# Kernel optimization log

Hardware: AMD Instinct MI355X
Metric: run time of the kernel (lower is better)

## Reference

```python
import jax, jax.numpy as jnp
import numpy as np

LATENT = 256
MID = 512
T = 5          # num_transforms
OUT = T * 6 + T  # 35
THRESH = 0.9   # MATRIX_NORM_THRESHOLD
EPS = 1e-5     # torch LayerNorm eps
B = 131072


def _xavier(key, fan_in, fan_out):
    lim = np.sqrt(6.0 / (fan_in + fan_out)).astype(np.float32)
    return jax.random.uniform(key, (fan_in, fan_out), jnp.float32, -lim, lim)


def setup_inputs() -> dict:
    key = jax.random.key(0)
    ks = jax.random.split(key, 8)
    z = jax.random.normal(ks[0], (B, LATENT), jnp.float32)
    W1 = _xavier(ks[1], LATENT, MID)
    Wa = _xavier(ks[2], MID, MID)
    Wb = _xavier(ks[3], MID, MID)
    Wout = _xavier(ks[4], MID, OUT)
    bias = lambda n: jnp.full((n,), 0.01, jnp.float32)  # nn.init.constant_(bias, 0.01)
    return {
        "z": z,
        "W1": W1, "b1": bias(MID), "g1": jnp.ones((MID,), jnp.float32), "be1": jnp.zeros((MID,), jnp.float32),
        "Wa": Wa, "ba": bias(MID), "ga": jnp.ones((MID,), jnp.float32), "bea": jnp.zeros((MID,), jnp.float32),
        "Wb": Wb, "bb": bias(MID), "gb": jnp.ones((MID,), jnp.float32), "beb": jnp.zeros((MID,), jnp.float32),
        "Wout": Wout, "bout": bias(OUT),
    }


def _layernorm(x, g, b):
    mu = jnp.mean(x, axis=-1, keepdims=True)
    var = jnp.mean(jnp.square(x - mu), axis=-1, keepdims=True)
    return (x - mu) * jax.lax.rsqrt(var + EPS) * g + b


def reference(z, W1, b1, g1, be1, Wa, ba, ga, bea, Wb, bb, gb, beb, Wout, bout):
    # Linear -> LayerNorm -> ReLU
    h = jax.nn.relu(_layernorm(z @ W1 + b1, g1, be1))
    # ResidualBlock: Linear -> LN -> SiLU -> Linear -> LN, then skip add
    y = jax.nn.silu(_layernorm(h @ Wa + ba, ga, bea))
    y = _layernorm(y @ Wb + bb, gb, beb)
    h = h + y
    x = h @ Wout + bout                     # [B, 35]

    affines = x[:, : T * 6].reshape(-1, T, 2, 3)  # [B, T, 2, 3]
    logits = x[:, T * 6:]                         # [B, T]
    probs = jax.nn.softmax(logits, axis=-1)

    M = affines[..., :2]                          # [B, T, 2, 2]
    U, S, Vh = jnp.linalg.svd(M, full_matrices=False)
    Sc = jnp.minimum(S, THRESH)                   # clamp(max=0.9)
    M2 = jnp.einsum("btij,btj,btjk->btik", U, Sc, Vh)
    affines = jnp.concatenate([M2, affines[..., 2:]], axis=-1)
    return affines, probs
```

## Files before the change

### kernel.cpp

```cpp
#include <hip/hip_runtime.h>
#include <hip/hip_bf16.h>

#define BQ     131072
#define NT     5

typedef unsigned short u16;
typedef unsigned int   u32;
typedef unsigned long long u64;
typedef __attribute__((ext_vector_type(8))) short bf16x8;
typedef __attribute__((ext_vector_type(4))) float f32x4;
typedef __attribute__((ext_vector_type(2))) float f32x2;

__device__ __forceinline__ u16 f2bf(float x) {
  union { float f; u32 u; } v; v.f = x;
  u32 r = (v.u + 0x7FFFu + ((v.u >> 16) & 1u)) >> 16;
  return (u16)r;
}

__global__ __launch_bounds__(256) void transpose_cast(
    const float* __restrict__ src, u16* __restrict__ dst, int K, int N, int NP) {
  __shared__ float tile[32][33];
  int kx = blockIdx.x * 32, ny = blockIdx.y * 32;
  int tx = threadIdx.x, ty = threadIdx.y;
#pragma unroll
  for (int i = 0; i < 4; i++) {
    int k = kx + ty + i * 8, n = ny + tx;
    tile[ty + i * 8][tx] = (k < K && n < N) ? src[(size_t)k * N + n] : 0.f;
  }
  __syncthreads();
#pragma unroll
  for (int i = 0; i < 4; i++) {
    int n = ny + ty + i * 8, k = kx + tx;
    if (n < NP && k < K) dst[(size_t)n * K + k] = f2bf(tile[tx][ty + i * 8]);
  }
}

template <int K, int ACT>
__device__ __forceinline__ void layer(
    const u16* __restrict__ wt, const float* __restrict__ bias,
    const float* __restrict__ gam, const float* __restrict__ bet,
    const u16* src, u16* dst, float* sStat,
    int lane, int wid, int l15, int lg, int wfb)
{
  f32x4 acc[2][4];
#pragma unroll
  for (int m = 0; m < 2; m++)
#pragma unroll
    for (int n = 0; n < 4; n++) acc[m][n] = (f32x4){0.f, 0.f, 0.f, 0.f};

#pragma unroll 2
  for (int kb = 0; kb < K; kb += 32) {
    const int k0 = kb + lg * 8;
    bf16x8 a[2];
#pragma unroll
    for (int m = 0; m < 2; m++)
      a[m] = *(const bf16x8*)(wt + (size_t)(wfb + m * 16 + l15) * K + k0);
    bf16x8 bv[4];
#pragma unroll
    for (int n = 0; n < 4; n++) {
      int b = n * 16 + l15;
      int byte = (b * (K * 2) + k0 * 2) ^ ((b & 7) << 4);
      bv[n] = *(const bf16x8*)((const char*)src + byte);
    }
    __builtin_amdgcn_s_setprio(1);
#pragma unroll
    for (int m = 0; m < 2; m++)
#pragma unroll
      for (int n = 0; n < 4; n++)
        acc[m][n] = __builtin_amdgcn_mfma_f32_16x16x32_bf16(a[m], bv[n], acc[m][n], 0, 0, 0);
    __builtin_amdgcn_s_setprio(0);
  }

#pragma unroll
  for (int m = 0; m < 2; m++) {
    f32x4 bv4 = *(const f32x4*)(bias + wfb + m * 16 + lg * 4);
#pragma unroll
    for (int n = 0; n < 4; n++)
#pragma unroll
      for (int r = 0; r < 4; r++) acc[m][n][r] += bv4[r];
  }

  float s[4], q[4];
#pragma unroll
  for (int n = 0; n < 4; n++) {
    s[n] = 0.f; q[n] = 0.f;
#pragma unroll
    for (int m = 0; m < 2; m++)
#pragma unroll
      for (int r = 0; r < 4; r++) { float v = acc[m][n][r]; s[n] += v; q[n] += v * v; }
    s[n] += __shfl_xor(s[n], 16); q[n] += __shfl_xor(q[n], 16);
    s[n] += __shfl_xor(s[n], 32); q[n] += __shfl_xor(q[n], 32);
  }
  if (lg == 0) {
#pragma unroll
    for (int n = 0; n < 4; n++) {
      int b = n * 16 + l15;
      *(f32x2*)(sStat + wid * 128 + b * 2) = (f32x2){s[n], q[n]};
    }
  }
  __syncthreads();

  float ss = 0.f, qq = 0.f;
#pragma unroll
  for (int w = 0; w < 16; w++) {
    f32x2 v = *(const f32x2*)(sStat + w * 128 + lane * 2);
    ss += v[0]; qq += v[1];
  }
  float meanb = ss * (1.f / 512.f);
  float rstdb = rsqrtf(qq * (1.f / 512.f) - meanb * meanb + 1e-5f);

  float mean[4], rstd[4];
#pragma unroll
  for (int n = 0; n < 4; n++) {
    mean[n] = __shfl(meanb, n * 16 + l15);
    rstd[n] = __shfl(rstdb, n * 16 + l15);
  }

#pragma unroll
  for (int m = 0; m < 2; m++) {
    int f0 = wfb + m * 16 + lg * 4;
    f32x4 gv  = *(const f32x4*)(gam + f0);
    f32x4 bev = *(const f32x4*)(bet + f0);
#pragma unroll
    for (int n = 0; n < 4; n++) {
      int b = n * 16 + l15;
      u16 pk[4];
#pragma unroll
      for (int r = 0; r < 4; r++) {
        float v = (acc[m][n][r] - mean[n]) * rstd[n] * gv[r] + bev[r];
        if (ACT == 1) v = fmaxf(v, 0.f);
        else if (ACT == 2) v = v / (1.f + __expf(-v));
        pk[r] = f2bf(v);
      }
      u64 w64 = (u64)pk[0] | ((u64)pk[1] << 16) | ((u64)pk[2] << 32) | ((u64)pk[3] << 48);
      int byte = (b * 1024 + f0 * 2) ^ ((b & 7) << 4);
      *(u64*)((char*)dst + byte) = w64;
    }
  }
  __syncthreads();
}

__global__ __launch_bounds__(1024) void ifs_main(
    const float* __restrict__ z,
    const u16* __restrict__ wt1, const u16* __restrict__ wta,
    const u16* __restrict__ wtb, const u16* __restrict__ wtout,
    const float* __restrict__ b1, const float* __restrict__ g1, const float* __restrict__ be1,
    const float* __restrict__ ba, const float* __restrict__ ga, const float* __restrict__ bea,
    const float* __restrict__ bb, const float* __restrict__ gb, const float* __restrict__ beb,
    const float* __restrict__ bout, float* __restrict__ out)
{
  __shared__ __align__(16) char smem[65536 * 2 + 8192];
  u16*   sA    = (u16*)smem;
  u16*   sB    = (u16*)(smem + 65536);
  float* sStat = (float*)(smem + 131072);

  const int tid  = threadIdx.x;
  const int lane = tid & 63, wid = tid >> 6;
  const int l15  = lane & 15, lg = lane >> 4;
  const int bbase = blockIdx.x * 64;
  const int wfb   = wid * 32;

#pragma unroll
  for (int i = 0; i < 4; i++) {
    int c = tid + i * 1024;
    int b = c >> 6, kc = c & 63;
    const float4 v = *(const float4*)(z + (size_t)(bbase + b) * 256 + kc * 4);
    u32 lo = (u32)f2bf(v.x) | ((u32)f2bf(v.y) << 16);
    u32 hi = (u32)f2bf(v.z) | ((u32)f2bf(v.w) << 16);
    u64 pk = (u64)lo | ((u64)hi << 32);
    int byte = (b * 512 + kc * 8) ^ ((b & 7) << 4);
    *(u64*)((char*)sB + byte) = pk;
  }
  __syncthreads();

  layer<256, 1>(wt1, b1, g1, be1, sB, sA, sStat, lane, wid, l15, lg, wfb);
  layer<512, 2>(wta, ba, ga, bea, sA, sB, sStat, lane, wid, l15, lg, wfb);
  layer<512, 0>(wtb, bb, gb, beb, sB, sB, sStat, lane, wid, l15, lg, wfb);

  {
    const int nf = wid & 3, kh = wid >> 2;
    const int b  = nf * 16 + l15;
    f32x4 xacc[3];
#pragma unroll
    for (int m = 0; m < 3; m++) xacc[m] = (f32x4){0.f, 0.f, 0.f, 0.f};
#pragma unroll 2
    for (int kk = 0; kk < 128; kk += 32) {
      int k0 = kh * 128 + kk + lg * 8;
      int byte = (b * 1024 + k0 * 2) ^ ((b & 7) << 4);
      bf16x8 bh = *(const bf16x8*)((const char*)sA + byte);
      bf16x8 by = *(const bf16x8*)((const char*)sB + byte);
#pragma unroll
      for (int m = 0; m < 3; m++) {
        bf16x8 aw = *(const bf16x8*)(wtout + (size_t)(m * 16 + l15) * 512 + k0);
        xacc[m] = __builtin_amdgcn_mfma_f32_16x16x32_bf16(aw, bh, xacc[m], 0, 0, 0);
        xacc[m] = __builtin_amdgcn_mfma_f32_16x16x32_bf16(aw, by, xacc[m], 0, 0, 0);
      }
    }
    __syncthreads();
    float* sP = (float*)sA;
#pragma unroll
    for (int m = 0; m < 3; m++)
      *(f32x4*)(sP + (size_t)(kh * 64 + b) * 48 + m * 16 + lg * 4) = xacc[m];
    __syncthreads();
    float* sX = (float*)sB;
    if (tid < 768) {
      int b2 = tid / 12, j = (tid - b2 * 12) * 4;
      f32x4 v0 = *(const f32x4*)(sP + (size_t)(0 * 64 + b2) * 48 + j);
      f32x4 v1 = *(const f32x4*)(sP + (size_t)(1 * 64 + b2) * 48 + j);
      f32x4 v2 = *(const f32x4*)(sP + (size_t)(2 * 64 + b2) * 48 + j);
      f32x4 v3 = *(const f32x4*)(sP + (size_t)(3 * 64 + b2) * 48 + j);
#pragma unroll
      for (int r = 0; r < 4; r++) v0[r] += v1[r] + v2[r] + v3[r];
      *(f32x4*)(sX + (size_t)b2 * 48 + j) = v0;
    }
    __syncthreads();

    if (tid < 64) {
      int bb2 = tid;
      float l[5], mx = -1e30f;
#pragma unroll
      for (int j = 0; j < 5; j++) { l[j] = sX[bb2 * 48 + 30 + j] + bout[30 + j]; mx = fmaxf(mx, l[j]); }
      float ssum = 0.f, e[5];
#pragma unroll
      for (int j = 0; j < 5; j++) { e[j] = __expf(l[j] - mx); ssum += e[j]; }
      float inv = 1.f / ssum;
      float* op = out + (size_t)BQ * 30 + (size_t)(bbase + bb2) * 5;
#pragma unroll
      for (int j = 0; j < 5; j++) op[j] = e[j] * inv;
    }
    if (tid < 320) {
      int b2 = tid / 5, t = tid - b2 * 5;
      const float* xr = sX + b2 * 48 + t * 6;
      float a   = xr[0] + bout[t * 6 + 0];
      float bb_ = xr[1] + bout[t * 6 + 1];
      float tx  = xr[2] + bout[t * 6 + 2];
      float c   = xr[3] + bout[t * 6 + 3];
      float d   = xr[4] + bout[t * 6 + 4];
      float ty  = xr[5] + bout[t * 6 + 5];
      float E = 0.5f * (a + d), F = 0.5f * (a - d);
      float G = 0.5f * (c + bb_), H = 0.5f * (c - bb_);
      float Q = sqrtf(E * E + H * H), R = sqrtf(F * F + G * G);
      float sx = Q + R, sy = Q - R;
      float a1 = atan2f(G, F), a2 = atan2f(H, E);
      float th = 0.5f * (a2 - a1), ph = 0.5f * (a2 + a1);
      float sxc = fminf(sx, 0.9f);
      float syc = fminf(fmaxf(sy, -0.9f), 0.9f);
      float st, ct, sp, cp;
      __sincosf(th, &st, &ct);
      __sincosf(ph, &sp, &cp);
      float ux = cp * sxc, uy = sp * sxc, vx = sp * syc, vy = cp * syc;
      float m00 =  ux * ct - vx * st;
      float m01 = -ux * st - vx * ct;
      float m10 =  uy * ct + vy * st;
      float m11 = -uy * st + vy * ct;
      float* op = out + (size_t)(bbase + b2) * 30 + t * 6;
      op[0] = m00; op[1] = m01; op[2] = tx;
      op[3] = m10; op[4] = m11; op[5] = ty;
    }
  }
}

extern "C" void kernel_launch(void* const* d_in, const int* in_sizes, int n_in,
                              void* d_out, int out_size, void* d_ws, size_t ws_size,
                              hipStream_t stream) {
  const float* z    = (const float*)d_in[0];
  const float* W1   = (const float*)d_in[1];
  const float* b1   = (const float*)d_in[2];
  const float* g1   = (const float*)d_in[3];
  const float* be1  = (const float*)d_in[4];
  const float* Wa   = (const float*)d_in[5];
  const float* ba   = (const float*)d_in[6];
  const float* ga   = (const float*)d_in[7];
  const float* bea  = (const float*)d_in[8];
  const float* Wb   = (const float*)d_in[9];
  const float* bb   = (const float*)d_in[10];
  const float* gb   = (const float*)d_in[11];
  const float* beb  = (const float*)d_in[12];
  const float* Wout = (const float*)d_in[13];
  const float* bout = (const float*)d_in[14];
  float* out = (float*)d_out;

  char* w = (char*)d_ws;
  u16* wt1   = (u16*)(w);
  u16* wta   = (u16*)(w + 262144);
  u16* wtb   = (u16*)(w + 786432);
  u16* wtout = (u16*)(w + 1310720);

  dim3 tb(32, 8);
  transpose_cast<<<dim3(8, 16),  tb, 0, stream>>>(W1,   wt1,   256, 512, 512);
  transpose_cast<<<dim3(16, 16), tb, 0, stream>>>(Wa,   wta,   512, 512, 512);
  transpose_cast<<<dim3(16, 16), tb, 0, stream>>>(Wb,   wtb,   512, 512, 512);
  transpose_cast<<<dim3(16, 2),  tb, 0, stream>>>(Wout, wtout, 512, 35,  48);

  ifs_main<<<BQ / 64, 1024, 0, stream>>>(
      z, wt1, wta, wtb, wtout,
      b1, g1, be1, ba, ga, bea, bb, gb, beb, bout, out);
}
```

Before: 658.6 us.

## Shrink main kernel to 32-row tiles with 8 waves and merge weight transposes

The fused MLP kernel now processes 32 batch rows per 512-thread block instead of 64 rows per 1024 threads. Each wave computes a 64-feature by 32-row tile, so weight-fragment loads per MFMA rise while activation loads fall. LDS per block drops to about 66 KB, and launch bounds ask for several blocks per CU to raise occupancy and overlap the layer barriers. The four weight transpose-cast launches are merged into one 3D-grid launch to cut launch overhead, but per-row weight reuse from global/L2 is halved.

New measurement: 852.3 us. +29.4%, slower.

```diff
diff --git a/kernel.cpp b/kernel.cpp
--- a/kernel.cpp
+++ b/kernel.cpp
@@ -3,6 +3,7 @@
 
 #define BQ     131072
 #define NT     5
+#define ROWS   32
 
 typedef unsigned short u16;
 typedef unsigned int   u32;
@@ -17,10 +18,20 @@
   return (u16)r;
 }
 
-__global__ __launch_bounds__(256) void transpose_cast(
-    const float* __restrict__ src, u16* __restrict__ dst, int K, int N, int NP) {
+__global__ __launch_bounds__(256) void transpose_cast_all(
+    const float* __restrict__ s0, const float* __restrict__ s1,
+    const float* __restrict__ s2, const float* __restrict__ s3,
+    u16* __restrict__ d0, u16* __restrict__ d1,
+    u16* __restrict__ d2, u16* __restrict__ d3) {
   __shared__ float tile[32][33];
+  const int z = blockIdx.z;
+  const float* src; u16* dst; int K, N, NP;
+  if      (z == 0) { src = s0; dst = d0; K = 256; N = 512; NP = 512; }
+  else if (z == 1) { src = s1; dst = d1; K = 512; N = 512; NP = 512; }
+  else if (z == 2) { src = s2; dst = d2; K = 512; N = 512; NP = 512; }
+  else             { src = s3; dst = d3; K = 512; N = 35;  NP = 48;  }
   int kx = blockIdx.x * 32, ny = blockIdx.y * 32;
+  if (kx >= K || ny >= NP) return;
   int tx = threadIdx.x, ty = threadIdx.y;
 #pragma unroll
   for (int i = 0; i < 4; i++) {
@@ -42,50 +53,50 @@
     const u16* src, u16* dst, float* sStat,
     int lane, int wid, int l15, int lg, int wfb)
 {
-  f32x4 acc[2][4];
-#pragma unroll
-  for (int m = 0; m < 2; m++)
-#pragma unroll
-    for (int n = 0; n < 4; n++) acc[m][n] = (f32x4){0.f, 0.f, 0.f, 0.f};
+  f32x4 acc[4][2];
+#pragma unroll
+  for (int m = 0; m < 4; m++)
+#pragma unroll
+    for (int n = 0; n < 2; n++) acc[m][n] = (f32x4){0.f, 0.f, 0.f, 0.f};
 
 #pragma unroll 2
   for (int kb = 0; kb < K; kb += 32) {
     const int k0 = kb + lg * 8;
-    bf16x8 a[2];
-#pragma unroll
-    for (int m = 0; m < 2; m++)
+    bf16x8 a[4];
+#pragma unroll
+    for (int m = 0; m < 4; m++)
       a[m] = *(const bf16x8*)(wt + (size_t)(wfb + m * 16 + l15) * K + k0);
-    bf16x8 bv[4];
-#pragma unroll
-    for (int n = 0; n < 4; n++) {
+    bf16x8 bv[2];
+#pragma unroll
+    for (int n = 0; n < 2; n++) {
       int b = n * 16 + l15;
       int byte = (b * (K * 2) + k0 * 2) ^ ((b & 7) << 4);
       bv[n] = *(const bf16x8*)((const char*)src + byte);
     }
     __builtin_amdgcn_s_setprio(1);
 #pragma unroll
-    for (int m = 0; m < 2; m++)
-#pragma unroll
-      for (int n = 0; n < 4; n++)
+    for (int m = 0; m < 4; m++)
+#pragma unroll
+      for (int n = 0; n < 2; n++)
         acc[m][n] = __builtin_amdgcn_mfma_f32_16x16x32_bf16(a[m], bv[n], acc[m][n], 0, 0, 0);
     __builtin_amdgcn_s_setprio(0);
   }
 
 #pragma unroll
-  for (int m = 0; m < 2; m++) {
+  for (int m = 0; m < 4; m++) {
     f32x4 bv4 = *(const f32x4*)(bias + wfb + m * 16 + lg * 4);
 #pragma unroll
-    for (int n = 0; n < 4; n++)
+    for (int n = 0; n < 2; n++)
 #pragma unroll
       for (int r = 0; r < 4; r++) acc[m][n][r] += bv4[r];
   }
 
-  float s[4], q[4];
-#pragma unroll
-  for (int n = 0; n < 4; n++) {
+  float s[2], q[2];
+#pragma unroll
+  for (int n = 0; n < 2; n++) {
     s[n] = 0.f; q[n] = 0.f;
 #pragma unroll
-    for (int m = 0; m < 2; m++)
+    for (int m = 0; m < 4; m++)
 #pragma unroll
       for (int r = 0; r < 4; r++) { float v = acc[m][n][r]; s[n] += v; q[n] += v * v; }
     s[n] += __shfl_xor(s[n], 16); q[n] += __shfl_xor(q[n], 16);
@@ -93,36 +104,37 @@
   }
   if (lg == 0) {
 #pragma unroll
-    for (int n = 0; n < 4; n++) {
+    for (int n = 0; n < 2; n++) {
       int b = n * 16 + l15;
-      *(f32x2*)(sStat + wid * 128 + b * 2) = (f32x2){s[n], q[n]};
+      *(f32x2*)(sStat + wid * 64 + b * 2) = (f32x2){s[n], q[n]};
     }
   }
   __syncthreads();
 
+  const int br = lane & 31;
   float ss = 0.f, qq = 0.f;
 #pragma unroll
-  for (int w = 0; w < 16; w++) {
-    f32x2 v = *(const f32x2*)(sStat + w * 128 + lane * 2);
+  for (int w = 0; w < 8; w++) {
+    f32x2 v = *(const f32x2*)(sStat + w * 64 + br * 2);
     ss += v[0]; qq += v[1];
   }
   float meanb = ss * (1.f / 512.f);
   float rstdb = rsqrtf(qq * (1.f / 512.f) - meanb * meanb + 1e-5f);
 
-  float mean[4], rstd[4];
-#pragma unroll
-  for (int n = 0; n < 4; n++) {
+  float mean[2], rstd[2];
+#pragma unroll
+  for (int n = 0; n < 2; n++) {
     mean[n] = __shfl(meanb, n * 16 + l15);
     rstd[n] = __shfl(rstdb, n * 16 + l15);
   }
 
 #pragma unroll
-  for (int m = 0; m < 2; m++) {
+  for (int m = 0; m < 4; m++) {
     int f0 = wfb + m * 16 + lg * 4;
     f32x4 gv  = *(const f32x4*)(gam + f0);
     f32x4 bev = *(const f32x4*)(bet + f0);
 #pragma unroll
-    for (int n = 0; n < 4; n++) {
+    for (int n = 0; n < 2; n++) {
       int b = n * 16 + l15;
       u16 pk[4];
 #pragma unroll
@@ -140,7 +152,7 @@
   __syncthreads();
 }
 
-__global__ __launch_bounds__(1024) void ifs_main(
+__global__ __launch_bounds__(512, 4) void ifs_main(
     const float* __restrict__ z,
     const u16* __restrict__ wt1, const u16* __restrict__ wta,
     const u16* __restrict__ wtb, const u16* __restrict__ wtout,
@@ -149,20 +161,20 @@
     const float* __restrict__ bb, const float* __restrict__ gb, const float* __restrict__ beb,
     const float* __restrict__ bout, float* __restrict__ out)
 {
-  __shared__ __align__(16) char smem[65536 * 2 + 8192];
+  __shared__ __align__(16) char smem[32768 * 2 + 2048];
   u16*   sA    = (u16*)smem;
-  u16*   sB    = (u16*)(smem + 65536);
-  float* sStat = (float*)(smem + 131072);
+  u16*   sB    = (u16*)(smem + 32768);
+  float* sStat = (float*)(smem + 65536);
 
   const int tid  = threadIdx.x;
   const int lane = tid & 63, wid = tid >> 6;
   const int l15  = lane & 15, lg = lane >> 4;
-  const int bbase = blockIdx.x * 64;
-  const int wfb   = wid * 32;
+  const int bbase = blockIdx.x * ROWS;
+  const int wfb   = wid * 64;
 
 #pragma unroll
   for (int i = 0; i < 4; i++) {
-    int c = tid + i * 1024;
+    int c = tid + i * 512;
     int b = c >> 6, kc = c & 63;
     const float4 v = *(const float4*)(z + (size_t)(bbase + b) * 256 + kc * 4);
     u32 lo = (u32)f2bf(v.x) | ((u32)f2bf(v.y) << 16);
@@ -178,7 +190,7 @@
   layer<512, 0>(wtb, bb, gb, beb, sB, sB, sStat, lane, wid, l15, lg, wfb);
 
   {
-    const int nf = wid & 3, kh = wid >> 2;
+    const int nf = wid & 1, kh = wid >> 1;
     const int b  = nf * 16 + l15;
     f32x4 xacc[3];
 #pragma unroll
@@ -200,22 +212,22 @@
     float* sP = (float*)sA;
 #pragma unroll
     for (int m = 0; m < 3; m++)
-      *(f32x4*)(sP + (size_t)(kh * 64 + b) * 48 + m * 16 + lg * 4) = xacc[m];
+      *(f32x4*)(sP + (size_t)(kh * 32 + b) * 48 + m * 16 + lg * 4) = xacc[m];
     __syncthreads();
     float* sX = (float*)sB;
-    if (tid < 768) {
+    if (tid < 384) {
       int b2 = tid / 12, j = (tid - b2 * 12) * 4;
-      f32x4 v0 = *(const f32x4*)(sP + (size_t)(0 * 64 + b2) * 48 + j);
-      f32x4 v1 = *(const f32x4*)(sP + (size_t)(1 * 64 + b2) * 48 + j);
-      f32x4 v2 = *(const f32x4*)(sP + (size_t)(2 * 64 + b2) * 48 + j);
-      f32x4 v3 = *(const f32x4*)(sP + (size_t)(3 * 64 + b2) * 48 + j);
+      f32x4 v0 = *(const f32x4*)(sP + (size_t)(0 * 32 + b2) * 48 + j);
+      f32x4 v1 = *(const f32x4*)(sP + (size_t)(1 * 32 + b2) * 48 + j);
+      f32x4 v2 = *(const f32x4*)(sP + (size_t)(2 * 32 + b2) * 48 + j);
+      f32x4 v3 = *(const f32x4*)(sP + (size_t)(3 * 32 + b2) * 48 + j);
 #pragma unroll
       for (int r = 0; r < 4; r++) v0[r] += v1[r] + v2[r] + v3[r];
       *(f32x4*)(sX + (size_t)b2 * 48 + j) = v0;
     }
     __syncthreads();
 
-    if (tid < 64) {
+    if (tid < ROWS) {
       int bb2 = tid;
       float l[5], mx = -1e30f;
 #pragma unroll
@@ -228,7 +240,7 @@
 #pragma unroll
       for (int j = 0; j < 5; j++) op[j] = e[j] * inv;
     }
-    if (tid < 320) {
+    if (tid < ROWS * NT) {
       int b2 = tid / 5, t = tid - b2 * 5;
       const float* xr = sX + b2 * 48 + t * 6;
       float a   = xr[0] + bout[t * 6 + 0];
@@ -286,13 +298,10 @@
   u16* wtb   = (u16*)(w + 786432);
   u16* wtout = (u16*)(w + 1310720);
 
-  dim3 tb(32, 8);
-  transpose_cast<<<dim3(8, 16),  tb, 0, stream>>>(W1,   wt1,   256, 512, 512);
-  transpose_cast<<<dim3(16, 16), tb, 0, stream>>>(Wa,   wta,   512, 512, 512);
-  transpose_cast<<<dim3(16, 16), tb, 0, stream>>>(Wb,   wtb,   512, 512, 512);
-  transpose_cast<<<dim3(16, 2),  tb, 0, stream>>>(Wout, wtout, 512, 35,  48);
-
-  ifs_main<<<BQ / 64, 1024, 0, stream>>>(
+  transpose_cast_all<<<dim3(16, 16, 4), dim3(32, 8), 0, stream>>>(
+      W1, Wa, Wb, Wout, wt1, wta, wtb, wtout);
+
+  ifs_main<<<BQ / ROWS, 512, 0, stream>>>(
       z, wt1, wta, wtb, wtout,
       b1, g1, be1, ba, ga, bea, bb, gb, beb, bout, out);
 }
```
